# Kernel tuning notes

Hardware: AMD Instinct MI355X
Metric: run time of the kernel (lower is better)

The kernel has to match this reference:

```python
import jax, jax.numpy as jnp
import numpy as np

DIM = 1024
HEADS = 16
DIM_HEAD = 64
INNER = HEADS * DIM_HEAD
B, N = 2, 2048


def setup_inputs() -> dict:
    key = jax.random.key(0)
    ks = jax.random.split(key, 5)
    x = jax.random.normal(ks[0], (B, N, DIM), dtype=jnp.float32)
    ln_gamma = jnp.ones((DIM,), dtype=jnp.float32)
    ln_beta = jnp.zeros((DIM,), dtype=jnp.float32)
    # torch Linear: weight [out, in]; store as [in, out] for x @ W
    W_qkv = jax.random.normal(ks[1], (DIM, 3 * INNER), dtype=jnp.float32) * (DIM ** -0.5)
    W_out = jax.random.normal(ks[2], (INNER, DIM), dtype=jnp.float32) * (INNER ** -0.5)
    b_out = jax.random.normal(ks[3], (DIM,), dtype=jnp.float32) * 0.01
    return {"x": x, "ln_gamma": ln_gamma, "ln_beta": ln_beta,
            "W_qkv": W_qkv, "W_out": W_out, "b_out": b_out}


def reference(x, ln_gamma, ln_beta, W_qkv, W_out, b_out):
    eps = 1e-5
    scale = DIM_HEAD ** -0.5
    # LayerNorm over last dim
    mu = jnp.mean(x, axis=-1, keepdims=True)
    var = jnp.mean((x - mu) ** 2, axis=-1, keepdims=True)
    xn = (x - mu) * jax.lax.rsqrt(var + eps) * ln_gamma + ln_beta
    # QKV projection (no bias), split
    qkv = xn @ W_qkv                               # [B, N, 3*inner]
    q, k, v = jnp.split(qkv, 3, axis=-1)           # each [B, N, inner]
    def heads(t):
        return t.reshape(B, N, HEADS, DIM_HEAD).transpose(0, 2, 1, 3)  # [B, H, N, d]
    q, k, v = heads(q), heads(k), heads(v)
    dots = jnp.einsum("bhnd,bhmd->bhnm", q, k) * scale
    a = jax.nn.softmax(dots, axis=-1)
    out = jnp.einsum("bhnm,bhmd->bhnd", a, v)      # [B, H, N, d]
    out = out.transpose(0, 2, 1, 3).reshape(B, N, INNER)
    return out @ W_out + b_out                     # dropout p=0 -> identity
```

## Files before the change

kernel.cpp:

```cpp
#include <hip/hip_runtime.h>

typedef unsigned short U16;
typedef __bf16 bf16x8 __attribute__((ext_vector_type(8)));
typedef float f32x4 __attribute__((ext_vector_type(4)));
typedef float f32x16 __attribute__((ext_vector_type(16)));

__device__ inline float b2f(U16 u) {
    union { unsigned int i; float f; } v;
    v.i = ((unsigned int)u) << 16;
    return v.f;
}
__device__ inline U16 f2b(float f) {
    union { float f; unsigned int u; } v;
    v.f = f;
    unsigned int r = (v.u + 0x7fffu + ((v.u >> 16) & 1u)) >> 16;
    return (U16)r;
}

__device__ inline unsigned cvt_pk(float lo, float hi) {
    unsigned d;
    asm("v_cvt_pk_bf16_f32 %0, %1, %2" : "=v"(d) : "v"(lo), "v"(hi));
    return d;
}
__device__ inline void plswap(unsigned &a, unsigned &b) {
    asm("v_permlane32_swap_b32 %0, %1" : "+v"(a), "+v"(b));
}

__device__ inline void gld16(const void* g, void* l) {
    __builtin_amdgcn_global_load_lds(
        (const __attribute__((address_space(1))) void*)g,
        (__attribute__((address_space(3))) void*)l, 16, 0, 0);
}

__global__ __launch_bounds__(256) void prep_kernel(const float* __restrict__ x,
                                                   const float* __restrict__ gamma,
                                                   const float* __restrict__ beta,
                                                   U16* __restrict__ xn,
                                                   const float* __restrict__ Wqkv,
                                                   U16* __restrict__ WqT,
                                                   const float* __restrict__ Wout,
                                                   U16* __restrict__ WoT) {
    int p = blockIdx.x;
    int t = threadIdx.x;
    if (p < 4096) {
        int row = p;
        float4 raw = ((const float4*)(x + (size_t)row * 1024))[t];
        float v[4] = { raw.x, raw.y, raw.z, raw.w };
        float s = v[0] + v[1] + v[2] + v[3];
        float s2 = v[0] * v[0] + v[1] * v[1] + v[2] * v[2] + v[3] * v[3];
#pragma unroll
        for (int off = 32; off >= 1; off >>= 1) {
            s  += __shfl_xor(s,  off);
            s2 += __shfl_xor(s2, off);
        }
        __shared__ float red[8];
        if ((t & 63) == 0) { red[(t >> 6) * 2] = s; red[(t >> 6) * 2 + 1] = s2; }
        __syncthreads();
        float S  = red[0] + red[2] + red[4] + red[6];
        float S2 = red[1] + red[3] + red[5] + red[7];
        float mu = S * (1.0f / 1024.0f);
        float var = S2 * (1.0f / 1024.0f) - mu * mu;
        float rstd = rsqrtf(var + 1e-5f);
        float4 g4 = ((const float4*)gamma)[t];
        float4 b4 = ((const float4*)beta)[t];
        ushort4 o;
        o.x = f2b((v[0] - mu) * rstd * g4.x + b4.x);
        o.y = f2b((v[1] - mu) * rstd * g4.y + b4.y);
        o.z = f2b((v[2] - mu) * rstd * g4.z + b4.z);
        o.w = f2b((v[3] - mu) * rstd * g4.w + b4.w);
        ((ushort4*)(xn + (size_t)row * 1024))[t] = o;
        return;
    }
    p -= 4096;
    const float* in; U16* out; int C, tilesx;
    if (p < 3072) { in = Wqkv; out = WqT; C = 3072; tilesx = 96; }
    else { p -= 3072; in = Wout; out = WoT; C = 1024; tilesx = 32; }
    const int R = 1024;
    int c0 = (p % tilesx) * 32, r0 = (p / tilesx) * 32;
    int tx = t & 31, ty = t >> 5;
    __shared__ float tile[32][33];
#pragma unroll
    for (int i = 0; i < 32; i += 8)
        tile[ty + i][tx] = in[(size_t)(r0 + ty + i) * C + c0 + tx];
    __syncthreads();
#pragma unroll
    for (int i = 0; i < 32; i += 8)
        out[(size_t)(c0 + ty + i) * R + r0 + tx] = f2b(tile[tx][ty + i]);
}

__global__ __launch_bounds__(512) void gemm256(const U16* __restrict__ A,
                                               const U16* __restrict__ Bt,
                                               U16* __restrict__ C,
                                               U16* __restrict__ vT,
                                               int M, int N, int K) {
    __shared__ __align__(16) U16 As[2][2][128 * 64];
    __shared__ __align__(16) U16 Bs[2][2][128 * 64];
    const int p = blockIdx.x;
    const int xcd = p & 7, sl = p >> 3;
    const int by = xcd * 2 + (sl >= 12 ? 1 : 0);
    const int bx = (sl >= 12) ? (sl - 12) : sl;
    const int m0 = by * 256, n0 = bx * 256;
    const int t = threadIdx.x;
    const int wave = t >> 6, lane = t & 63, l15 = lane & 15, quad = lane >> 4;
    const int wm = wave >> 2, wn = wave & 3;

    f32x4 acc[8][4];
#pragma unroll
    for (int i = 0; i < 8; i++)
#pragma unroll
        for (int j = 0; j < 4; j++)
            acc[i][j] = (f32x4){0.f, 0.f, 0.f, 0.f};

    const int c0 = t, c1 = 512 + t;
    const int sr0 = c0 >> 3, so0 = (c0 & 7) ^ (sr0 & 7);
    const int sr1 = c1 >> 3, so1 = (c1 & 7) ^ (sr1 & 7);
    const U16* Ag0 = A + (size_t)(m0 + sr0) * K + so0 * 8;
    const U16* Ag1 = A + (size_t)(m0 + sr1) * K + so1 * 8;
    const U16* Bg0 = Bt + (size_t)(n0 + sr0) * K + so0 * 8;
    const U16* Bg1 = Bt + (size_t)(n0 + sr1) * K + so1 * 8;
    const size_t hstep = (size_t)128 * K;

    auto stA = [&](int kt, U16* d0, U16* d1) {
        gld16(Ag0 + kt * 64, d0 + c0 * 8);
        gld16(Ag1 + kt * 64, d0 + c1 * 8);
        gld16(Ag0 + hstep + kt * 64, d1 + c0 * 8);
        gld16(Ag1 + hstep + kt * 64, d1 + c1 * 8);
    };
    auto stB = [&](int kt, U16* d0, U16* d1) {
        gld16(Bg0 + kt * 64, d0 + c0 * 8);
        gld16(Bg1 + kt * 64, d0 + c1 * 8);
        gld16(Bg0 + hstep + kt * 64, d1 + c0 * 8);
        gld16(Bg1 + hstep + kt * 64, d1 + c1 * 8);
    };

    const int slot0 = quad ^ (l15 & 7);
    const int slot1 = (4 + quad) ^ (l15 & 7);
    const int aoff0 = l15 * 64 + slot0 * 8, aoff1 = l15 * 64 + slot1 * 8;
    const int bbase = (wn & 1) * 64 * 64;
    const int boff0 = bbase + aoff0, boff1 = bbase + aoff1;
    const int nk = K >> 6;

    auto ktile = [&](const U16* Ac0, const U16* Ac1, const U16* Bc0, const U16* Bc1,
                     U16* An0, U16* An1, U16* Bn0, U16* Bn1, int kt) {
        const bool nx = (kt + 1) < nk;
        if (nx) {
            stA(kt + 1, An0, An1);
            asm volatile("s_waitcnt vmcnt(4)" ::: "memory");
        } else {
            asm volatile("s_waitcnt vmcnt(0)" ::: "memory");
        }
        __builtin_amdgcn_s_barrier();
        asm volatile("" ::: "memory");
        const U16* Ah = wm ? Ac1 : Ac0;
        const U16* Bh = (wn & 2) ? Bc1 : Bc0;
        bf16x8 bfr[4][2], af[4][2];
#pragma unroll
        for (int j = 0; j < 4; j++) {
            bfr[j][0] = *(const bf16x8*)&Bh[j * 16 * 64 + boff0];
            bfr[j][1] = *(const bf16x8*)&Bh[j * 16 * 64 + boff1];
        }
#pragma unroll
        for (int i = 0; i < 4; i++) {
            af[i][0] = *(const bf16x8*)&Ah[i * 16 * 64 + aoff0];
            af[i][1] = *(const bf16x8*)&Ah[i * 16 * 64 + aoff1];
        }
        if (nx) stB(kt + 1, Bn0, Bn1);
        __builtin_amdgcn_s_setprio(1);
#pragma unroll
        for (int i = 0; i < 4; i++)
#pragma unroll
            for (int j = 0; j < 4; j++) {
                acc[i][j] = __builtin_amdgcn_mfma_f32_16x16x32_bf16(af[i][0], bfr[j][0], acc[i][j], 0, 0, 0);
                acc[i][j] = __builtin_amdgcn_mfma_f32_16x16x32_bf16(af[i][1], bfr[j][1], acc[i][j], 0, 0, 0);
            }
        __builtin_amdgcn_s_setprio(0);
        asm volatile("" ::: "memory");
        __builtin_amdgcn_s_barrier();
        asm volatile("" ::: "memory");
#pragma unroll
        for (int i = 0; i < 4; i++) {
            af[i][0] = *(const bf16x8*)&Ah[(4 + i) * 16 * 64 + aoff0];
            af[i][1] = *(const bf16x8*)&Ah[(4 + i) * 16 * 64 + aoff1];
        }
        __builtin_amdgcn_s_setprio(1);
#pragma unroll
        for (int i = 0; i < 4; i++)
#pragma unroll
            for (int j = 0; j < 4; j++) {
                acc[4 + i][j] = __builtin_amdgcn_mfma_f32_16x16x32_bf16(af[i][0], bfr[j][0], acc[4 + i][j], 0, 0, 0);
                acc[4 + i][j] = __builtin_amdgcn_mfma_f32_16x16x32_bf16(af[i][1], bfr[j][1], acc[4 + i][j], 0, 0, 0);
            }
        __builtin_amdgcn_s_setprio(0);
        asm volatile("" ::: "memory");
        __builtin_amdgcn_s_barrier();
        asm volatile("" ::: "memory");
    };

    stA(0, &As[0][0][0], &As[0][1][0]);
    stB(0, &Bs[0][0][0], &Bs[0][1][0]);
    asm volatile("s_waitcnt vmcnt(0)" ::: "memory");
    __builtin_amdgcn_s_barrier();
    asm volatile("" ::: "memory");

    for (int kt = 0; kt < nk; kt += 2) {
        ktile(&As[0][0][0], &As[0][1][0], &Bs[0][0][0], &Bs[0][1][0],
              &As[1][0][0], &As[1][1][0], &Bs[1][0][0], &Bs[1][1][0], kt);
        ktile(&As[1][0][0], &As[1][1][0], &Bs[1][0][0], &Bs[1][1][0],
              &As[0][0][0], &As[0][1][0], &Bs[0][0][0], &Bs[0][1][0], kt + 1);
    }

    if (vT && n0 >= 2048) {
#pragma unroll
        for (int i = 0; i < 8; i++) {
#pragma unroll
            for (int j = 0; j < 4; j++) {
                int col = n0 + wn * 64 + j * 16 + l15 - 2048;
                int hh = col >> 6, dd = col & 63;
                int row0 = m0 + wm * 128 + i * 16 + quad * 4;
                int bb = row0 >> 11, nn = row0 & 2047;
                ushort4 st;
                st.x = f2b(acc[i][j][0]); st.y = f2b(acc[i][j][1]);
                st.z = f2b(acc[i][j][2]); st.w = f2b(acc[i][j][3]);
                *(ushort4*)&vT[((((size_t)bb * 16) + hh) * 64 + dd) * 2048 + nn] = st;
            }
        }
        return;
    }
#pragma unroll
    for (int i = 0; i < 8; i++) {
#pragma unroll
        for (int j = 0; j < 4; j++) {
            int col = n0 + wn * 64 + j * 16 + l15;
#pragma unroll
            for (int r = 0; r < 4; r++) {
                int row = m0 + wm * 128 + i * 16 + quad * 4 + r;
                C[(size_t)row * N + col] = f2b(acc[i][j][r]);
            }
        }
    }
}

__global__ __launch_bounds__(256) void gemm_bt2(const U16* __restrict__ A,
                                                const U16* __restrict__ Bt,
                                                const float* __restrict__ bias,
                                                float* __restrict__ C,
                                                int M, int N, int K) {
    __shared__ __align__(16) U16 As[64 * 32];
    __shared__ __align__(16) U16 Bs[128 * 32];
    const int m0 = blockIdx.y * 64, n0 = blockIdx.x * 128;
    const int t = threadIdx.x;
    const int wave = t >> 6, lane = t & 63, l15 = lane & 15, quad = lane >> 4;
    const int wm = (wave >> 1) * 32, wn = (wave & 1) * 64;

    f32x4 acc[2][4];
#pragma unroll
    for (int i = 0; i < 2; i++)
#pragma unroll
        for (int j = 0; j < 4; j++)
            acc[i][j] = (f32x4){0.f, 0.f, 0.f, 0.f};

    const int rA = t >> 2, kqA = t & 3;

    for (int k0 = 0; k0 < K; k0 += 32) {
        gld16(&A[(size_t)(m0 + rA) * K + k0 + kqA * 8], &As[t * 8]);
        gld16(&Bt[(size_t)(n0 + rA) * K + k0 + kqA * 8], &Bs[t * 8]);
        gld16(&Bt[(size_t)(n0 + 64 + rA) * K + k0 + kqA * 8], &Bs[(256 + t) * 8]);
        __syncthreads();
        bf16x8 af[2], bfr[4];
#pragma unroll
        for (int i = 0; i < 2; i++)
            af[i] = *(const bf16x8*)&As[(wm + i * 16 + l15) * 32 + quad * 8];
#pragma unroll
        for (int j = 0; j < 4; j++)
            bfr[j] = *(const bf16x8*)&Bs[(wn + j * 16 + l15) * 32 + quad * 8];
#pragma unroll
        for (int i = 0; i < 2; i++)
#pragma unroll
            for (int j = 0; j < 4; j++)
                acc[i][j] = __builtin_amdgcn_mfma_f32_16x16x32_bf16(
                    af[i], bfr[j], acc[i][j], 0, 0, 0);
        __syncthreads();
    }
#pragma unroll
    for (int i = 0; i < 2; i++) {
#pragma unroll
        for (int j = 0; j < 4; j++) {
            int col = n0 + wn + j * 16 + l15;
            float bv = bias[col];
#pragma unroll
            for (int r = 0; r < 4; r++) {
                int row = m0 + wm + i * 16 + quad * 4 + r;
                C[(size_t)row * N + col] = acc[i][j][r] + bv;
            }
        }
    }
}

__global__ __launch_bounds__(256) void attn_kernel(const U16* __restrict__ qkv,
                                                   const U16* __restrict__ vT,
                                                   U16* __restrict__ attn_out) {
    const int p = blockIdx.x;
    const int xcd = p & 7;
    const int slot = p >> 3;
    const int bh = ((slot & 3) << 3) | xcd;
    const int qt = slot >> 2;
    const int b = bh >> 4, h = bh & 15;
    const int t = threadIdx.x;
    const int wave = t >> 6, lane = t & 63;
    const int l31 = lane & 31, hi = lane >> 5;
    const float sc2 = 0.125f * 1.44269504089f;

    __shared__ __align__(16) U16 Kt[2][64 * 64];
    __shared__ __align__(16) U16 Vt[2][64 * 64];

    const size_t base = (size_t)(b * 2048) * 3072;
    const U16* vTbh = vT + ((size_t)(b * 16 + h) * 64) * 2048;

    bf16x8 qf[4];
    {
        int qrow = qt * 128 + wave * 32 + l31;
        const U16* qp = qkv + base + (size_t)qrow * 3072 + h * 64 + hi * 8;
#pragma unroll
        for (int s = 0; s < 4; s++) {
            union { bf16x8 v; U16 u[8]; } a;
            a.v = *(const bf16x8*)&qp[s * 16];
#pragma unroll
            for (int e = 0; e < 8; e++) a.u[e] = f2b(b2f(a.u[e]) * sc2);
            qf[s] = a.v;
        }
    }

    float l4[4] = { 0.f, 0.f, 0.f, 0.f };
    f32x16 oacc[2];
#pragma unroll
    for (int db = 0; db < 2; db++)
#pragma unroll
        for (int r = 0; r < 16; r++)
            oacc[db][r] = 0.0f;

    const int c0 = t, c1 = 256 + t;
    const int row0 = c0 >> 3, oct0 = (c0 & 7) ^ (row0 & 7);
    const int row1 = c1 >> 3, oct1 = (c1 & 7) ^ (row1 & 7);

    gld16(&qkv[base + (size_t)row0 * 3072 + 1024 + h * 64 + oct0 * 8], &Kt[0][c0 * 8]);
    gld16(&qkv[base + (size_t)row1 * 3072 + 1024 + h * 64 + oct1 * 8], &Kt[0][c1 * 8]);
    gld16(&vTbh[(size_t)row0 * 2048 + oct0 * 8], &Vt[0][c0 * 8]);
    gld16(&vTbh[(size_t)row1 * 2048 + oct1 * 8], &Vt[0][c1 * 8]);
    __syncthreads();

    auto step = [&](const U16* KtC, const U16* VtC, U16* KtN, U16* VtN, int nt) {
        gld16(&qkv[base + (size_t)(nt * 64 + row0) * 3072 + 1024 + h * 64 + oct0 * 8], &KtN[c0 * 8]);
        gld16(&qkv[base + (size_t)(nt * 64 + row1) * 3072 + 1024 + h * 64 + oct1 * 8], &KtN[c1 * 8]);
        gld16(&vTbh[(size_t)row0 * 2048 + nt * 64 + oct0 * 8], &VtN[c0 * 8]);
        gld16(&vTbh[(size_t)row1 * 2048 + nt * 64 + oct1 * 8], &VtN[c1 * 8]);
#pragma unroll
        for (int kb = 0; kb < 2; kb++) {
            bf16x8 kf[4];
#pragma unroll
            for (int s = 0; s < 4; s++)
                kf[s] = *(const bf16x8*)&KtC[(kb * 32 + l31) * 64 +
                                             (((s * 2 + hi) ^ (l31 & 7)) * 8)];
            bf16x8 vfr[2][2];
#pragma unroll
            for (int db = 0; db < 2; db++)
#pragma unroll
                for (int s = 0; s < 2; s++)
                    vfr[db][s] = *(const bf16x8*)&VtC[(db * 32 + l31) * 64 +
                                                      (((kb * 4 + s * 2 + hi) ^ (l31 & 7)) * 8)];

            f32x16 st = {0.f, 0.f, 0.f, 0.f, 0.f, 0.f, 0.f, 0.f,
                         0.f, 0.f, 0.f, 0.f, 0.f, 0.f, 0.f, 0.f};
            __builtin_amdgcn_s_setprio(1);
#pragma unroll
            for (int s = 0; s < 4; s++)
                st = __builtin_amdgcn_mfma_f32_32x32x16_bf16(kf[s], qf[s], st, 0, 0, 0);
            __builtin_amdgcn_s_setprio(0);

            float pe[16];
#pragma unroll
            for (int r = 0; r < 16; r++) {
                pe[r] = __builtin_amdgcn_exp2f(st[r]);
                l4[r & 3] += pe[r];
            }

#pragma unroll
            for (int s = 0; s < 2; s++) {
                unsigned p01 = cvt_pk(pe[s * 8 + 0], pe[s * 8 + 1]);
                unsigned p23 = cvt_pk(pe[s * 8 + 2], pe[s * 8 + 3]);
                unsigned p45 = cvt_pk(pe[s * 8 + 4], pe[s * 8 + 5]);
                unsigned p67 = cvt_pk(pe[s * 8 + 6], pe[s * 8 + 7]);
                plswap(p01, p45);
                plswap(p23, p67);
                union { unsigned u[4]; bf16x8 v; } pw;
                pw.u[0] = p01; pw.u[1] = p23; pw.u[2] = p45; pw.u[3] = p67;
                __builtin_amdgcn_s_setprio(1);
#pragma unroll
                for (int db = 0; db < 2; db++)
                    oacc[db] = __builtin_amdgcn_mfma_f32_32x32x16_bf16(
                        vfr[db][s], pw.v, oacc[db], 0, 0, 0);
                __builtin_amdgcn_s_setprio(0);
            }
        }
        __syncthreads();
    };

    for (int kt2 = 0; kt2 < 16; kt2++) {
        step(&Kt[0][0], &Vt[0][0], &Kt[1][0], &Vt[1][0], 2 * kt2 + 1);
        step(&Kt[1][0], &Vt[1][0], &Kt[0][0], &Vt[0][0], (2 * kt2 + 2) & 31);
    }

    float l_acc = (l4[0] + l4[1]) + (l4[2] + l4[3]);
    float lt = l_acc + __shfl_xor(l_acc, 32);
    float inv = 1.0f / lt;
    int qrow = b * 2048 + qt * 128 + wave * 32 + l31;
#pragma unroll
    for (int db = 0; db < 2; db++) {
#pragma unroll
        for (int g = 0; g < 4; g++) {
            ushort4 stv;
            stv.x = f2b(oacc[db][g * 4 + 0] * inv);
            stv.y = f2b(oacc[db][g * 4 + 1] * inv);
            stv.z = f2b(oacc[db][g * 4 + 2] * inv);
            stv.w = f2b(oacc[db][g * 4 + 3] * inv);
            int col = h * 64 + db * 32 + g * 8 + hi * 4;
            *(ushort4*)&attn_out[(size_t)qrow * 1024 + col] = stv;
        }
    }
}

extern "C" void kernel_launch(void* const* d_in, const int* in_sizes, int n_in,
                              void* d_out, int out_size, void* d_ws, size_t ws_size,
                              hipStream_t stream) {
    (void)in_sizes; (void)n_in; (void)out_size; (void)ws_size;
    const float* x    = (const float*)d_in[0];
    const float* g    = (const float*)d_in[1];
    const float* be   = (const float*)d_in[2];
    const float* Wqkv = (const float*)d_in[3];
    const float* Wout = (const float*)d_in[4];
    const float* bout = (const float*)d_in[5];
    float* out = (float*)d_out;
    char* ws = (char*)d_ws;

    U16* xn   = (U16*)(ws);
    U16* qkv  = (U16*)(ws + (size_t)(8u  << 20));
    U16* WqT  = (U16*)(ws + (size_t)(32u << 20));
    U16* WoT  = (U16*)(ws + (size_t)(38u << 20));
    U16* vT   = (U16*)(ws + (size_t)(40u << 20));
    U16* aout = xn;

    prep_kernel<<<8192, 256, 0, stream>>>(x, g, be, xn, Wqkv, WqT, Wout, WoT);
    gemm256<<<192, 512, 0, stream>>>(xn, WqT, qkv, vT, 4096, 3072, 1024);
    attn_kernel<<<512, 256, 0, stream>>>(qkv, vT, aout);
    gemm_bt2<<<dim3(1024 / 128, 4096 / 64), 256, 0, stream>>>(aout, WoT, bout, out, 4096, 1024, 1024);
}
```

Before: 193.4 us.

## Double-buffer output-projection GEMM and interleave attention score/PV MFMA chains

```diff
diff --git a/kernel.cpp b/kernel.cpp
--- a/kernel.cpp
+++ b/kernel.cpp
@@ -245,8 +245,8 @@
                                                 const float* __restrict__ bias,
                                                 float* __restrict__ C,
                                                 int M, int N, int K) {
-    __shared__ __align__(16) U16 As[64 * 32];
-    __shared__ __align__(16) U16 Bs[128 * 32];
+    __shared__ __align__(16) U16 As[2][64 * 64];
+    __shared__ __align__(16) U16 Bs[2][128 * 64];
     const int m0 = blockIdx.y * 64, n0 = blockIdx.x * 128;
     const int t = threadIdx.x;
     const int wave = t >> 6, lane = t & 63, l15 = lane & 15, quad = lane >> 4;
@@ -259,28 +259,83 @@
         for (int j = 0; j < 4; j++)
             acc[i][j] = (f32x4){0.f, 0.f, 0.f, 0.f};
 
-    const int rA = t >> 2, kqA = t & 3;
-
-    for (int k0 = 0; k0 < K; k0 += 32) {
-        gld16(&A[(size_t)(m0 + rA) * K + k0 + kqA * 8], &As[t * 8]);
-        gld16(&Bt[(size_t)(n0 + rA) * K + k0 + kqA * 8], &Bs[t * 8]);
-        gld16(&Bt[(size_t)(n0 + 64 + rA) * K + k0 + kqA * 8], &Bs[(256 + t) * 8]);
-        __syncthreads();
-        bf16x8 af[2], bfr[4];
+    const int cA0 = t, cA1 = 256 + t;
+    const int srA0 = cA0 >> 3, soA0 = (cA0 & 7) ^ (srA0 & 7);
+    const int srA1 = cA1 >> 3, soA1 = (cA1 & 7) ^ (srA1 & 7);
+    const U16* AgA0 = A + (size_t)(m0 + srA0) * K + soA0 * 8;
+    const U16* AgA1 = A + (size_t)(m0 + srA1) * K + soA1 * 8;
+    const int cB0 = t, cB1 = 256 + t, cB2 = 512 + t, cB3 = 768 + t;
+    const int srB0 = cB0 >> 3, soB0 = (cB0 & 7) ^ (srB0 & 7);
+    const int srB1 = cB1 >> 3, soB1 = (cB1 & 7) ^ (srB1 & 7);
+    const int srB2 = cB2 >> 3, soB2 = (cB2 & 7) ^ (srB2 & 7);
+    const int srB3 = cB3 >> 3, soB3 = (cB3 & 7) ^ (srB3 & 7);
+    const U16* BgB0 = Bt + (size_t)(n0 + srB0) * K + soB0 * 8;
+    const U16* BgB1 = Bt + (size_t)(n0 + srB1) * K + soB1 * 8;
+    const U16* BgB2 = Bt + (size_t)(n0 + srB2) * K + soB2 * 8;
+    const U16* BgB3 = Bt + (size_t)(n0 + srB3) * K + soB3 * 8;
+
+    auto stAf = [&](int kt, U16* d) {
+        gld16(AgA0 + kt * 64, d + cA0 * 8);
+        gld16(AgA1 + kt * 64, d + cA1 * 8);
+    };
+    auto stBf = [&](int kt, U16* d) {
+        gld16(BgB0 + kt * 64, d + cB0 * 8);
+        gld16(BgB1 + kt * 64, d + cB1 * 8);
+        gld16(BgB2 + kt * 64, d + cB2 * 8);
+        gld16(BgB3 + kt * 64, d + cB3 * 8);
+    };
+
+    const int as0 = (quad ^ (l15 & 7)) * 8;
+    const int as1 = ((4 + quad) ^ (l15 & 7)) * 8;
+    const int nk = K >> 6;
+
+    auto ktile = [&](const U16* Ac, const U16* Bc, U16* An, U16* Bn, int kt) {
+        const bool nx = (kt + 1) < nk;
+        if (nx) {
+            stAf(kt + 1, An);
+            asm volatile("s_waitcnt vmcnt(2)" ::: "memory");
+        } else {
+            asm volatile("s_waitcnt vmcnt(0)" ::: "memory");
+        }
+        __builtin_amdgcn_s_barrier();
+        asm volatile("" ::: "memory");
+        bf16x8 af[2][2], bfr[4][2];
+#pragma unroll
+        for (int i = 0; i < 2; i++) {
+            af[i][0] = *(const bf16x8*)&Ac[(wm + i * 16 + l15) * 64 + as0];
+            af[i][1] = *(const bf16x8*)&Ac[(wm + i * 16 + l15) * 64 + as1];
+        }
+#pragma unroll
+        for (int j = 0; j < 4; j++) {
+            bfr[j][0] = *(const bf16x8*)&Bc[(wn + j * 16 + l15) * 64 + as0];
+            bfr[j][1] = *(const bf16x8*)&Bc[(wn + j * 16 + l15) * 64 + as1];
+        }
+        if (nx) stBf(kt + 1, Bn);
+        __builtin_amdgcn_s_setprio(1);
 #pragma unroll
         for (int i = 0; i < 2; i++)
-            af[i] = *(const bf16x8*)&As[(wm + i * 16 + l15) * 32 + quad * 8];
-#pragma unroll
-        for (int j = 0; j < 4; j++)
-            bfr[j] = *(const bf16x8*)&Bs[(wn + j * 16 + l15) * 32 + quad * 8];
-#pragma unroll
-        for (int i = 0; i < 2; i++)
-#pragma unroll
-            for (int j = 0; j < 4; j++)
-                acc[i][j] = __builtin_amdgcn_mfma_f32_16x16x32_bf16(
-                    af[i], bfr[j], acc[i][j], 0, 0, 0);
-        __syncthreads();
-    }
+#pragma unroll
+            for (int j = 0; j < 4; j++) {
+                acc[i][j] = __builtin_amdgcn_mfma_f32_16x16x32_bf16(af[i][0], bfr[j][0], acc[i][j], 0, 0, 0);
+                acc[i][j] = __builtin_amdgcn_mfma_f32_16x16x32_bf16(af[i][1], bfr[j][1], acc[i][j], 0, 0, 0);
+            }
+        __builtin_amdgcn_s_setprio(0);
+        asm volatile("" ::: "memory");
+        __builtin_amdgcn_s_barrier();
+        asm volatile("" ::: "memory");
+    };
+
+    stAf(0, &As[0][0]);
+    stBf(0, &Bs[0][0]);
+    asm volatile("s_waitcnt vmcnt(0)" ::: "memory");
+    __builtin_amdgcn_s_barrier();
+    asm volatile("" ::: "memory");
+
+    for (int kt = 0; kt < nk; kt += 2) {
+        ktile(&As[0][0], &Bs[0][0], &As[1][0], &Bs[1][0], kt);
+        ktile(&As[1][0], &Bs[1][0], &As[0][0], &Bs[0][0], kt + 1);
+    }
+
 #pragma unroll
     for (int i = 0; i < 2; i++) {
 #pragma unroll
@@ -331,12 +386,14 @@
     }
 
     float l4[4] = { 0.f, 0.f, 0.f, 0.f };
-    f32x16 oacc[2];
+    f32x16 oaccA[2], oaccB[2];
 #pragma unroll
     for (int db = 0; db < 2; db++)
 #pragma unroll
-        for (int r = 0; r < 16; r++)
-            oacc[db][r] = 0.0f;
+        for (int r = 0; r < 16; r++) {
+            oaccA[db][r] = 0.0f;
+            oaccB[db][r] = 0.0f;
+        }
 
     const int c0 = t, c1 = 256 + t;
     const int row0 = c0 >> 3, oct0 = (c0 & 7) ^ (row0 & 7);
@@ -353,53 +410,83 @@
         gld16(&qkv[base + (size_t)(nt * 64 + row1) * 3072 + 1024 + h * 64 + oct1 * 8], &KtN[c1 * 8]);
         gld16(&vTbh[(size_t)row0 * 2048 + nt * 64 + oct0 * 8], &VtN[c0 * 8]);
         gld16(&vTbh[(size_t)row1 * 2048 + nt * 64 + oct1 * 8], &VtN[c1 * 8]);
-#pragma unroll
-        for (int kb = 0; kb < 2; kb++) {
-            bf16x8 kf[4];
+
+        bf16x8 kf[2][4];
+#pragma unroll
+        for (int kb = 0; kb < 2; kb++)
 #pragma unroll
             for (int s = 0; s < 4; s++)
-                kf[s] = *(const bf16x8*)&KtC[(kb * 32 + l31) * 64 +
-                                             (((s * 2 + hi) ^ (l31 & 7)) * 8)];
-            bf16x8 vfr[2][2];
+                kf[kb][s] = *(const bf16x8*)&KtC[(kb * 32 + l31) * 64 +
+                                                 (((s * 2 + hi) ^ (l31 & 7)) * 8)];
+        bf16x8 vfr[2][2][2];
+#pragma unroll
+        for (int kb = 0; kb < 2; kb++)
 #pragma unroll
             for (int db = 0; db < 2; db++)
 #pragma unroll
                 for (int s = 0; s < 2; s++)
-                    vfr[db][s] = *(const bf16x8*)&VtC[(db * 32 + l31) * 64 +
-                                                      (((kb * 4 + s * 2 + hi) ^ (l31 & 7)) * 8)];
-
-            f32x16 st = {0.f, 0.f, 0.f, 0.f, 0.f, 0.f, 0.f, 0.f,
-                         0.f, 0.f, 0.f, 0.f, 0.f, 0.f, 0.f, 0.f};
+                    vfr[kb][db][s] = *(const bf16x8*)&VtC[(db * 32 + l31) * 64 +
+                                                          (((kb * 4 + s * 2 + hi) ^ (l31 & 7)) * 8)];
+
+        f32x16 stA = {0.f, 0.f, 0.f, 0.f, 0.f, 0.f, 0.f, 0.f,
+                      0.f, 0.f, 0.f, 0.f, 0.f, 0.f, 0.f, 0.f};
+        f32x16 stB = stA;
+        __builtin_amdgcn_s_setprio(1);
+#pragma unroll
+        for (int s = 0; s < 4; s++)
+            stA = __builtin_amdgcn_mfma_f32_32x32x16_bf16(kf[0][s], qf[s], stA, 0, 0, 0);
+#pragma unroll
+        for (int s = 0; s < 4; s++)
+            stB = __builtin_amdgcn_mfma_f32_32x32x16_bf16(kf[1][s], qf[s], stB, 0, 0, 0);
+        __builtin_amdgcn_s_setprio(0);
+
+        {
+            float pe[16];
+#pragma unroll
+            for (int r = 0; r < 16; r++) {
+                pe[r] = __builtin_amdgcn_exp2f(stA[r]);
+                l4[r & 3] += pe[r];
+            }
+            unsigned p01 = cvt_pk(pe[0], pe[1]), p23 = cvt_pk(pe[2], pe[3]);
+            unsigned p45 = cvt_pk(pe[4], pe[5]), p67 = cvt_pk(pe[6], pe[7]);
+            plswap(p01, p45); plswap(p23, p67);
+            union { unsigned u[4]; bf16x8 v; } pw0;
+            pw0.u[0] = p01; pw0.u[1] = p23; pw0.u[2] = p45; pw0.u[3] = p67;
+            unsigned q01 = cvt_pk(pe[8], pe[9]), q23 = cvt_pk(pe[10], pe[11]);
+            unsigned q45 = cvt_pk(pe[12], pe[13]), q67 = cvt_pk(pe[14], pe[15]);
+            plswap(q01, q45); plswap(q23, q67);
+            union { unsigned u[4]; bf16x8 v; } pw1;
+            pw1.u[0] = q01; pw1.u[1] = q23; pw1.u[2] = q45; pw1.u[3] = q67;
             __builtin_amdgcn_s_setprio(1);
-#pragma unroll
-            for (int s = 0; s < 4; s++)
-                st = __builtin_amdgcn_mfma_f32_32x32x16_bf16(kf[s], qf[s], st, 0, 0, 0);
+            oaccA[0] = __builtin_amdgcn_mfma_f32_32x32x16_bf16(vfr[0][0][0], pw0.v, oaccA[0], 0, 0, 0);
+            oaccA[1] = __builtin_amdgcn_mfma_f32_32x32x16_bf16(vfr[0][1][0], pw0.v, oaccA[1], 0, 0, 0);
+            oaccB[0] = __builtin_amdgcn_mfma_f32_32x32x16_bf16(vfr[0][0][1], pw1.v, oaccB[0], 0, 0, 0);
+            oaccB[1] = __builtin_amdgcn_mfma_f32_32x32x16_bf16(vfr[0][1][1], pw1.v, oaccB[1], 0, 0, 0);
             __builtin_amdgcn_s_setprio(0);
-
+        }
+        {
             float pe[16];
 #pragma unroll
             for (int r = 0; r < 16; r++) {
-                pe[r] = __builtin_amdgcn_exp2f(st[r]);
+                pe[r] = __builtin_amdgcn_exp2f(stB[r]);
                 l4[r & 3] += pe[r];
             }
-
-#pragma unroll
-            for (int s = 0; s < 2; s++) {
-                unsigned p01 = cvt_pk(pe[s * 8 + 0], pe[s * 8 + 1]);
-                unsigned p23 = cvt_pk(pe[s * 8 + 2], pe[s * 8 + 3]);
-                unsigned p45 = cvt_pk(pe[s * 8 + 4], pe[s * 8 + 5]);
-                unsigned p67 = cvt_pk(pe[s * 8 + 6], pe[s * 8 + 7]);
-                plswap(p01, p45);
-                plswap(p23, p67);
-                union { unsigned u[4]; bf16x8 v; } pw;
-                pw.u[0] = p01; pw.u[1] = p23; pw.u[2] = p45; pw.u[3] = p67;
-                __builtin_amdgcn_s_setprio(1);
-#pragma unroll
-                for (int db = 0; db < 2; db++)
-                    oacc[db] = __builtin_amdgcn_mfma_f32_32x32x16_bf16(
-                        vfr[db][s], pw.v, oacc[db], 0, 0, 0);
-                __builtin_amdgcn_s_setprio(0);
-            }
+            unsigned p01 = cvt_pk(pe[0], pe[1]), p23 = cvt_pk(pe[2], pe[3]);
+            unsigned p45 = cvt_pk(pe[4], pe[5]), p67 = cvt_pk(pe[6], pe[7]);
+            plswap(p01, p45); plswap(p23, p67);
+            union { unsigned u[4]; bf16x8 v; } pw0;
+            pw0.u[0] = p01; pw0.u[1] = p23; pw0.u[2] = p45; pw0.u[3] = p67;
+            unsigned q01 = cvt_pk(pe[8], pe[9]), q23 = cvt_pk(pe[10], pe[11]);
+            unsigned q45 = cvt_pk(pe[12], pe[13]), q67 = cvt_pk(pe[14], pe[15]);
+            plswap(q01, q45); plswap(q23, q67);
+            union { unsigned u[4]; bf16x8 v; } pw1;
+            pw1.u[0] = q01; pw1.u[1] = q23; pw1.u[2] = q45; pw1.u[3] = q67;
+            __builtin_amdgcn_s_setprio(1);
+            oaccA[0] = __builtin_amdgcn_mfma_f32_32x32x16_bf16(vfr[1][0][0], pw0.v, oaccA[0], 0, 0, 0);
+            oaccA[1] = __builtin_amdgcn_mfma_f32_32x32x16_bf16(vfr[1][1][0], pw0.v, oaccA[1], 0, 0, 0);
+            oaccB[0] = __builtin_amdgcn_mfma_f32_32x32x16_bf16(vfr[1][0][1], pw1.v, oaccB[0], 0, 0, 0);
+            oaccB[1] = __builtin_amdgcn_mfma_f32_32x32x16_bf16(vfr[1][1][1], pw1.v, oaccB[1], 0, 0, 0);
+            __builtin_amdgcn_s_setprio(0);
         }
         __syncthreads();
     };
@@ -415,13 +502,14 @@
     int qrow = b * 2048 + qt * 128 + wave * 32 + l31;
 #pragma unroll
     for (int db = 0; db < 2; db++) {
+        f32x16 o = oaccA[db] + oaccB[db];
 #pragma unroll
         for (int g = 0; g < 4; g++) {
             ushort4 stv;
-            stv.x = f2b(oacc[db][g * 4 + 0] * inv);
-            stv.y = f2b(oacc[db][g * 4 + 1] * inv);
-            stv.z = f2b(oacc[db][g * 4 + 2] * inv);
-            stv.w = f2b(oacc[db][g * 4 + 3] * inv);
+            stv.x = f2b(o[g * 4 + 0] * inv);
+            stv.y = f2b(o[g * 4 + 1] * inv);
+            stv.z = f2b(o[g * 4 + 2] * inv);
+            stv.w = f2b(o[g * 4 + 3] * inv);
             int col = h * 64 + db * 32 + g * 8 + hi * 4;
             *(ushort4*)&attn_out[(size_t)qrow * 1024 + col] = stv;
         }
```

New measurement: 191.2 us. No clear change (-1.2%).

## Retile QKV GEMM to 256x192 and pipeline output GEMM with swizzled double buffering

Applied to the files above, without the earlier changes.

```diff
diff --git a/kernel.cpp b/kernel.cpp
--- a/kernel.cpp
+++ b/kernel.cpp
@@ -88,27 +88,27 @@
         out[(size_t)(c0 + ty + i) * R + r0 + tx] = f2b(tile[tx][ty + i]);
 }
 
-__global__ __launch_bounds__(512) void gemm256(const U16* __restrict__ A,
+__global__ __launch_bounds__(512) void gemm_g1(const U16* __restrict__ A,
                                                const U16* __restrict__ Bt,
                                                U16* __restrict__ C,
                                                U16* __restrict__ vT,
                                                int M, int N, int K) {
     __shared__ __align__(16) U16 As[2][2][128 * 64];
-    __shared__ __align__(16) U16 Bs[2][2][128 * 64];
+    __shared__ __align__(16) U16 Bs[2][192 * 64];
     const int p = blockIdx.x;
     const int xcd = p & 7, sl = p >> 3;
-    const int by = xcd * 2 + (sl >= 12 ? 1 : 0);
-    const int bx = (sl >= 12) ? (sl - 12) : sl;
-    const int m0 = by * 256, n0 = bx * 256;
+    const int by = xcd * 2 + (sl >> 4);
+    const int bx = sl & 15;
+    const int m0 = by * 256, n0 = bx * 192;
     const int t = threadIdx.x;
     const int wave = t >> 6, lane = t & 63, l15 = lane & 15, quad = lane >> 4;
     const int wm = wave >> 2, wn = wave & 3;
 
-    f32x4 acc[8][4];
+    f32x4 acc[8][3];
 #pragma unroll
     for (int i = 0; i < 8; i++)
 #pragma unroll
-        for (int j = 0; j < 4; j++)
+        for (int j = 0; j < 3; j++)
             acc[i][j] = (f32x4){0.f, 0.f, 0.f, 0.f};
 
     const int c0 = t, c1 = 512 + t;
@@ -116,9 +116,13 @@
     const int sr1 = c1 >> 3, so1 = (c1 & 7) ^ (sr1 & 7);
     const U16* Ag0 = A + (size_t)(m0 + sr0) * K + so0 * 8;
     const U16* Ag1 = A + (size_t)(m0 + sr1) * K + so1 * 8;
+    const size_t hstep = (size_t)128 * K;
+
+    const int cb2 = 1024 + t;
+    const int sb2 = cb2 >> 3, ob2 = (cb2 & 7) ^ (sb2 & 7);
     const U16* Bg0 = Bt + (size_t)(n0 + sr0) * K + so0 * 8;
     const U16* Bg1 = Bt + (size_t)(n0 + sr1) * K + so1 * 8;
-    const size_t hstep = (size_t)128 * K;
+    const U16* Bg2 = Bt + (size_t)(n0 + sb2) * K + ob2 * 8;
 
     auto stA = [&](int kt, U16* d0, U16* d1) {
         gld16(Ag0 + kt * 64, d0 + c0 * 8);
@@ -126,22 +130,20 @@
         gld16(Ag0 + hstep + kt * 64, d1 + c0 * 8);
         gld16(Ag1 + hstep + kt * 64, d1 + c1 * 8);
     };
-    auto stB = [&](int kt, U16* d0, U16* d1) {
-        gld16(Bg0 + kt * 64, d0 + c0 * 8);
-        gld16(Bg1 + kt * 64, d0 + c1 * 8);
-        gld16(Bg0 + hstep + kt * 64, d1 + c0 * 8);
-        gld16(Bg1 + hstep + kt * 64, d1 + c1 * 8);
+    auto stB = [&](int kt, U16* d) {
+        gld16(Bg0 + kt * 64, d + c0 * 8);
+        gld16(Bg1 + kt * 64, d + c1 * 8);
+        gld16(Bg2 + kt * 64, d + cb2 * 8);
     };
 
     const int slot0 = quad ^ (l15 & 7);
     const int slot1 = (4 + quad) ^ (l15 & 7);
     const int aoff0 = l15 * 64 + slot0 * 8, aoff1 = l15 * 64 + slot1 * 8;
-    const int bbase = (wn & 1) * 64 * 64;
-    const int boff0 = bbase + aoff0, boff1 = bbase + aoff1;
+    const int boff0 = wn * 48 * 64 + aoff0, boff1 = wn * 48 * 64 + aoff1;
     const int nk = K >> 6;
 
-    auto ktile = [&](const U16* Ac0, const U16* Ac1, const U16* Bc0, const U16* Bc1,
-                     U16* An0, U16* An1, U16* Bn0, U16* Bn1, int kt) {
+    auto ktile = [&](const U16* Ac0, const U16* Ac1, const U16* Bc,
+                     U16* An0, U16* An1, U16* Bn, int kt) {
         const bool nx = (kt + 1) < nk;
         if (nx) {
             stA(kt + 1, An0, An1);
@@ -152,24 +154,23 @@
         __builtin_amdgcn_s_barrier();
         asm volatile("" ::: "memory");
         const U16* Ah = wm ? Ac1 : Ac0;
-        const U16* Bh = (wn & 2) ? Bc1 : Bc0;
-        bf16x8 bfr[4][2], af[4][2];
-#pragma unroll
-        for (int j = 0; j < 4; j++) {
-            bfr[j][0] = *(const bf16x8*)&Bh[j * 16 * 64 + boff0];
-            bfr[j][1] = *(const bf16x8*)&Bh[j * 16 * 64 + boff1];
+        bf16x8 bfr[3][2], af[4][2];
+#pragma unroll
+        for (int j = 0; j < 3; j++) {
+            bfr[j][0] = *(const bf16x8*)&Bc[j * 16 * 64 + boff0];
+            bfr[j][1] = *(const bf16x8*)&Bc[j * 16 * 64 + boff1];
         }
 #pragma unroll
         for (int i = 0; i < 4; i++) {
             af[i][0] = *(const bf16x8*)&Ah[i * 16 * 64 + aoff0];
             af[i][1] = *(const bf16x8*)&Ah[i * 16 * 64 + aoff1];
         }
-        if (nx) stB(kt + 1, Bn0, Bn1);
+        if (nx) stB(kt + 1, Bn);
         __builtin_amdgcn_s_setprio(1);
 #pragma unroll
         for (int i = 0; i < 4; i++)
 #pragma unroll
-            for (int j = 0; j < 4; j++) {
+            for (int j = 0; j < 3; j++) {
                 acc[i][j] = __builtin_amdgcn_mfma_f32_16x16x32_bf16(af[i][0], bfr[j][0], acc[i][j], 0, 0, 0);
                 acc[i][j] = __builtin_amdgcn_mfma_f32_16x16x32_bf16(af[i][1], bfr[j][1], acc[i][j], 0, 0, 0);
             }
@@ -186,7 +187,7 @@
 #pragma unroll
         for (int i = 0; i < 4; i++)
 #pragma unroll
-            for (int j = 0; j < 4; j++) {
+            for (int j = 0; j < 3; j++) {
                 acc[4 + i][j] = __builtin_amdgcn_mfma_f32_16x16x32_bf16(af[i][0], bfr[j][0], acc[4 + i][j], 0, 0, 0);
                 acc[4 + i][j] = __builtin_amdgcn_mfma_f32_16x16x32_bf16(af[i][1], bfr[j][1], acc[4 + i][j], 0, 0, 0);
             }
@@ -197,24 +198,25 @@
     };
 
     stA(0, &As[0][0][0], &As[0][1][0]);
-    stB(0, &Bs[0][0][0], &Bs[0][1][0]);
+    stB(0, &Bs[0][0]);
     asm volatile("s_waitcnt vmcnt(0)" ::: "memory");
     __builtin_amdgcn_s_barrier();
     asm volatile("" ::: "memory");
 
     for (int kt = 0; kt < nk; kt += 2) {
-        ktile(&As[0][0][0], &As[0][1][0], &Bs[0][0][0], &Bs[0][1][0],
-              &As[1][0][0], &As[1][1][0], &Bs[1][0][0], &Bs[1][1][0], kt);
-        ktile(&As[1][0][0], &As[1][1][0], &Bs[1][0][0], &Bs[1][1][0],
-              &As[0][0][0], &As[0][1][0], &Bs[0][0][0], &Bs[0][1][0], kt + 1);
-    }
-
-    if (vT && n0 >= 2048) {
-#pragma unroll
-        for (int i = 0; i < 8; i++) {
-#pragma unroll
-            for (int j = 0; j < 4; j++) {
-                int col = n0 + wn * 64 + j * 16 + l15 - 2048;
+        ktile(&As[0][0][0], &As[0][1][0], &Bs[0][0],
+              &As[1][0][0], &As[1][1][0], &Bs[1][0], kt);
+        ktile(&As[1][0][0], &As[1][1][0], &Bs[1][0],
+              &As[0][0][0], &As[0][1][0], &Bs[0][0], kt + 1);
+    }
+
+#pragma unroll
+    for (int j = 0; j < 3; j++) {
+        int cb = n0 + wn * 48 + j * 16;
+        if (vT && cb >= 2048) {
+#pragma unroll
+            for (int i = 0; i < 8; i++) {
+                int col = cb + l15 - 2048;
                 int hh = col >> 6, dd = col & 63;
                 int row0 = m0 + wm * 128 + i * 16 + quad * 4;
                 int bb = row0 >> 11, nn = row0 & 2047;
@@ -223,18 +225,14 @@
                 st.z = f2b(acc[i][j][2]); st.w = f2b(acc[i][j][3]);
                 *(ushort4*)&vT[((((size_t)bb * 16) + hh) * 64 + dd) * 2048 + nn] = st;
             }
-        }
-        return;
-    }
-#pragma unroll
-    for (int i = 0; i < 8; i++) {
-#pragma unroll
-        for (int j = 0; j < 4; j++) {
-            int col = n0 + wn * 64 + j * 16 + l15;
-#pragma unroll
-            for (int r = 0; r < 4; r++) {
-                int row = m0 + wm * 128 + i * 16 + quad * 4 + r;
-                C[(size_t)row * N + col] = f2b(acc[i][j][r]);
+        } else {
+#pragma unroll
+            for (int i = 0; i < 8; i++) {
+                int col = cb + l15;
+                int row0 = m0 + wm * 128 + i * 16 + quad * 4;
+#pragma unroll
+                for (int r = 0; r < 4; r++)
+                    C[(size_t)(row0 + r) * N + col] = f2b(acc[i][j][r]);
             }
         }
     }
@@ -245,8 +243,8 @@
                                                 const float* __restrict__ bias,
                                                 float* __restrict__ C,
                                                 int M, int N, int K) {
-    __shared__ __align__(16) U16 As[64 * 32];
-    __shared__ __align__(16) U16 Bs[128 * 32];
+    __shared__ __align__(16) U16 As[2][64 * 64];
+    __shared__ __align__(16) U16 Bs[2][128 * 64];
     const int m0 = blockIdx.y * 64, n0 = blockIdx.x * 128;
     const int t = threadIdx.x;
     const int wave = t >> 6, lane = t & 63, l15 = lane & 15, quad = lane >> 4;
@@ -259,28 +257,83 @@
         for (int j = 0; j < 4; j++)
             acc[i][j] = (f32x4){0.f, 0.f, 0.f, 0.f};
 
-    const int rA = t >> 2, kqA = t & 3;
-
-    for (int k0 = 0; k0 < K; k0 += 32) {
-        gld16(&A[(size_t)(m0 + rA) * K + k0 + kqA * 8], &As[t * 8]);
-        gld16(&Bt[(size_t)(n0 + rA) * K + k0 + kqA * 8], &Bs[t * 8]);
-        gld16(&Bt[(size_t)(n0 + 64 + rA) * K + k0 + kqA * 8], &Bs[(256 + t) * 8]);
-        __syncthreads();
-        bf16x8 af[2], bfr[4];
+    const int cA0 = t, cA1 = 256 + t;
+    const int srA0 = cA0 >> 3, soA0 = (cA0 & 7) ^ (srA0 & 7);
+    const int srA1 = cA1 >> 3, soA1 = (cA1 & 7) ^ (srA1 & 7);
+    const U16* AgA0 = A + (size_t)(m0 + srA0) * K + soA0 * 8;
+    const U16* AgA1 = A + (size_t)(m0 + srA1) * K + soA1 * 8;
+    const int cB0 = t, cB1 = 256 + t, cB2 = 512 + t, cB3 = 768 + t;
+    const int srB0 = cB0 >> 3, soB0 = (cB0 & 7) ^ (srB0 & 7);
+    const int srB1 = cB1 >> 3, soB1 = (cB1 & 7) ^ (srB1 & 7);
+    const int srB2 = cB2 >> 3, soB2 = (cB2 & 7) ^ (srB2 & 7);
+    const int srB3 = cB3 >> 3, soB3 = (cB3 & 7) ^ (srB3 & 7);
+    const U16* BgB0 = Bt + (size_t)(n0 + srB0) * K + soB0 * 8;
+    const U16* BgB1 = Bt + (size_t)(n0 + srB1) * K + soB1 * 8;
+    const U16* BgB2 = Bt + (size_t)(n0 + srB2) * K + soB2 * 8;
+    const U16* BgB3 = Bt + (size_t)(n0 + srB3) * K + soB3 * 8;
+
+    auto stAf = [&](int kt, U16* d) {
+        gld16(AgA0 + kt * 64, d + cA0 * 8);
+        gld16(AgA1 + kt * 64, d + cA1 * 8);
+    };
+    auto stBf = [&](int kt, U16* d) {
+        gld16(BgB0 + kt * 64, d + cB0 * 8);
+        gld16(BgB1 + kt * 64, d + cB1 * 8);
+        gld16(BgB2 + kt * 64, d + cB2 * 8);
+        gld16(BgB3 + kt * 64, d + cB3 * 8);
+    };
+
+    const int as0 = (quad ^ (l15 & 7)) * 8;
+    const int as1 = ((4 + quad) ^ (l15 & 7)) * 8;
+    const int nk = K >> 6;
+
+    auto ktile = [&](const U16* Ac, const U16* Bc, U16* An, U16* Bn, int kt) {
+        const bool nx = (kt + 1) < nk;
+        if (nx) {
+            stAf(kt + 1, An);
+            asm volatile("s_waitcnt vmcnt(2)" ::: "memory");
+        } else {
+            asm volatile("s_waitcnt vmcnt(0)" ::: "memory");
+        }
+        __builtin_amdgcn_s_barrier();
+        asm volatile("" ::: "memory");
+        bf16x8 af[2][2], bfr[4][2];
+#pragma unroll
+        for (int i = 0; i < 2; i++) {
+            af[i][0] = *(const bf16x8*)&Ac[(wm + i * 16 + l15) * 64 + as0];
+            af[i][1] = *(const bf16x8*)&Ac[(wm + i * 16 + l15) * 64 + as1];
+        }
+#pragma unroll
+        for (int j = 0; j < 4; j++) {
+            bfr[j][0] = *(const bf16x8*)&Bc[(wn + j * 16 + l15) * 64 + as0];
+            bfr[j][1] = *(const bf16x8*)&Bc[(wn + j * 16 + l15) * 64 + as1];
+        }
+        if (nx) stBf(kt + 1, Bn);
+        __builtin_amdgcn_s_setprio(1);
 #pragma unroll
         for (int i = 0; i < 2; i++)
-            af[i] = *(const bf16x8*)&As[(wm + i * 16 + l15) * 32 + quad * 8];
-#pragma unroll
-        for (int j = 0; j < 4; j++)
-            bfr[j] = *(const bf16x8*)&Bs[(wn + j * 16 + l15) * 32 + quad * 8];
-#pragma unroll
-        for (int i = 0; i < 2; i++)
-#pragma unroll
-            for (int j = 0; j < 4; j++)
-                acc[i][j] = __builtin_amdgcn_mfma_f32_16x16x32_bf16(
-                    af[i], bfr[j], acc[i][j], 0, 0, 0);
-        __syncthreads();
-    }
+#pragma unroll
+            for (int j = 0; j < 4; j++) {
+                acc[i][j] = __builtin_amdgcn_mfma_f32_16x16x32_bf16(af[i][0], bfr[j][0], acc[i][j], 0, 0, 0);
+                acc[i][j] = __builtin_amdgcn_mfma_f32_16x16x32_bf16(af[i][1], bfr[j][1], acc[i][j], 0, 0, 0);
+            }
+        __builtin_amdgcn_s_setprio(0);
+        asm volatile("" ::: "memory");
+        __builtin_amdgcn_s_barrier();
+        asm volatile("" ::: "memory");
+    };
+
+    stAf(0, &As[0][0]);
+    stBf(0, &Bs[0][0]);
+    asm volatile("s_waitcnt vmcnt(0)" ::: "memory");
+    __builtin_amdgcn_s_barrier();
+    asm volatile("" ::: "memory");
+
+    for (int kt = 0; kt < nk; kt += 2) {
+        ktile(&As[0][0], &Bs[0][0], &As[1][0], &Bs[1][0], kt);
+        ktile(&As[1][0], &Bs[1][0], &As[0][0], &Bs[0][0], kt + 1);
+    }
+
 #pragma unroll
     for (int i = 0; i < 2; i++) {
 #pragma unroll
@@ -449,7 +502,7 @@
     U16* aout = xn;
 
     prep_kernel<<<8192, 256, 0, stream>>>(x, g, be, xn, Wqkv, WqT, Wout, WoT);
-    gemm256<<<192, 512, 0, stream>>>(xn, WqT, qkv, vT, 4096, 3072, 1024);
+    gemm_g1<<<256, 512, 0, stream>>>(xn, WqT, qkv, vT, 4096, 3072, 1024);
     attn_kernel<<<512, 256, 0, stream>>>(qkv, vT, aout);
     gemm_bt2<<<dim3(1024 / 128, 4096 / 64), 256, 0, stream>>>(aout, WoT, bout, out, 4096, 1024, 1024);
 }
```

Result: faster. 181.0 us (-6.4%).
